# Optimization experiments

Measured on AMD Instinct MI355X. Metric: run time of the kernel, lower is better.

## Reference

```python
import jax, jax.numpy as jnp
import numpy as np

LN_EPS = 1e-5
NEG = -1e9


def _layernorm(x, g, b):
    m = jnp.mean(x, axis=-1, keepdims=True)
    v = jnp.mean(jnp.square(x - m), axis=-1, keepdims=True)
    return (x - m) * jax.lax.rsqrt(v + LN_EPS) * g + b


def setup_inputs() -> dict:
    key = jax.random.key(0)
    ks = jax.random.split(key, 16)
    B, S, E, H, D = 4, 2048, 1024, 16, 64
    s = 0.02
    return {
        "x": jax.random.normal(ks[0], (B, S, E), jnp.float32),
        "mask": jax.random.randint(ks[1], (B, S), 0, 2, jnp.int32),
        "Wq": jax.random.normal(ks[2], (H, E, D), jnp.float32) * s,
        "bq": jnp.zeros((H, D), jnp.float32),
        "Wk": jax.random.normal(ks[3], (H, E, D), jnp.float32) * s,
        "bk": jnp.zeros((H, D), jnp.float32),
        "Wv": jax.random.normal(ks[4], (H, E, D), jnp.float32) * s,
        "bv": jnp.zeros((H, D), jnp.float32),
        "Wo": jax.random.normal(ks[5], (H * D, E), jnp.float32) * s,
        "bo": jnp.zeros((E,), jnp.float32),
        "g1": jnp.ones((E,), jnp.float32),
        "b1": jnp.zeros((E,), jnp.float32),
        "W1": jax.random.normal(ks[6], (E, D), jnp.float32) * s,
        "c1": jnp.zeros((D,), jnp.float32),
        "W2": jax.random.normal(ks[7], (D, E), jnp.float32) * s,
        "c2": jnp.zeros((E,), jnp.float32),
        "g2": jnp.ones((E,), jnp.float32),
        "b2": jnp.zeros((E,), jnp.float32),
    }


def reference(x, mask, Wq, bq, Wk, bk, Wv, bv, Wo, bo, g1, b1, W1, c1, W2, c2, g2, b2):
    B, S, E = x.shape
    # per-head projections, batched over heads: [B,H,S,D]
    q = jnp.einsum('bse,hed->bhsd', x, Wq) + bq[None, :, None, :]
    k = jnp.einsum('bse,hed->bhsd', x, Wk) + bk[None, :, None, :]
    v = jnp.einsum('bse,hed->bhsd', x, Wv) + bv[None, :, None, :]
    # NOTE: original scales by sqrt(seq_len) (query.size(1)), not sqrt(head_dim)
    scale = jnp.asarray(S, x.dtype) ** 0.5
    scores = jnp.einsum('bhsd,bhtd->bhst', q, k) / scale
    scores = jnp.where(mask[:, None, None, :] == 0, NEG, scores)
    attn = jax.nn.softmax(scores, axis=-1)
    ctx = jnp.einsum('bhst,bhtd->bhsd', attn, v)
    # concat heads: [B,S,H*D]
    ctx = ctx.transpose(0, 2, 1, 3).reshape(B, S, -1)
    h = _layernorm(ctx @ Wo + bo, g1, b1)
    # bottleneck FFN (dropout = identity at eval), exact GELU
    f = jax.nn.gelu(h @ W1 + c1, approximate=False) @ W2 + c2
    # no residual connection in the original module
    return _layernorm(f, g2, b2)
```

## Files before the change

### kernel.cpp

```cpp
#include <hip/hip_runtime.h>
#include <math.h>

#define B_ 4
#define S_ 2048
#define E_ 1024
#define H_ 16
#define D_ 64
#define M_ (B_*S_)
#define QSCALE (0.022097086912079608f * 1.4426950408889634f)

typedef __bf16 bf16_t;
typedef __bf16 bf16x8 __attribute__((ext_vector_type(8)));
typedef float  f32x4  __attribute__((ext_vector_type(4)));

__device__ __forceinline__ void gload_lds16(const void* g, void* l) {
    __builtin_amdgcn_global_load_lds(
        (const __attribute__((address_space(1))) void*)g,
        (__attribute__((address_space(3))) void*)l, 16, 0, 0);
}
__device__ __forceinline__ bf16x8 ldsx8(const void* p) {
    return __builtin_bit_cast(bf16x8, *(const uint4*)p);
}
__device__ __forceinline__ unsigned short bf16bits(float x) {
    return __builtin_bit_cast(unsigned short, (bf16_t)x);
}
__device__ __forceinline__ int fk(int row) { return ((row & 3) + 2 * ((row >> 3) & 3)) & 7; }

template<int BM, int BN, int MODE>
__global__ __launch_bounds__(256) void gemm_bf16(
    const bf16_t* __restrict__ A, const bf16_t* __restrict__ Bt,
    bf16_t* __restrict__ ob0, bf16_t* __restrict__ ob1, bf16_t* __restrict__ ob2,
    const float* __restrict__ bias0, const float* __restrict__ bias1,
    const int* __restrict__ sidx, const int* __restrict__ nkv,
    int M, int N, int K)
{
    constexpr int FM = BM / 32, FN = BN / 32;
    __shared__ bf16_t As[BM * 64];
    __shared__ bf16_t Bs[BN * 64];

    const int tid = threadIdx.x;
    const int w   = tid >> 6;
    const int wr  = w >> 1, wc = w & 1;
    const int lr  = tid & 15;
    const int lg  = (tid >> 4) & 3;

    const int nwg  = gridDim.x * gridDim.y;
    int bidf = blockIdx.y * gridDim.x + blockIdx.x;
    bidf = (bidf & 7) * (nwg >> 3) + (bidf >> 3);
    const int bm = (bidf / gridDim.x) * BM;
    const int bn = (bidf % gridDim.x) * BN;

    int arow[FM];
    if constexpr (MODE == 2) {
        const int b2 = bm >> 11, rbase = bm & 2047;
        const int nkp128 = (nkv[b2] + 127) & ~127;
        if (rbase >= nkp128) return;
        #pragma unroll
        for (int i = 0; i < FM; ++i) {
            const int row = (i * 256 + tid) >> 3;
            arow[i] = (b2 << 11) + sidx[(b2 << 11) + rbase + row];
        }
    }

    f32x4 acc[FM][FN] = {};

    for (int kk = 0; kk < K; kk += 64) {
        __syncthreads();
        #pragma unroll
        for (int i = 0; i < BM / 32; ++i) {
            int idx = i * 256 + tid;
            int row = idx >> 3, slot = idx & 7;
            const size_t grow = (MODE == 2) ? (size_t)arow[i] : (size_t)(bm + row);
            gload_lds16(A + grow * K + kk + (slot ^ (row & 7)) * 8,
                        (char*)As + idx * 16);
        }
        #pragma unroll
        for (int i = 0; i < BN / 32; ++i) {
            int idx = i * 256 + tid;
            int row = idx >> 3, slot = idx & 7;
            gload_lds16(Bt + (size_t)(bn + row) * K + kk + (slot ^ (row & 7)) * 8,
                        (char*)Bs + idx * 16);
        }
        __syncthreads();

        #pragma unroll
        for (int h = 0; h < 2; ++h) {
            bf16x8 af[FM], bfr[FN];
            #pragma unroll
            for (int m = 0; m < FM; ++m) {
                int row = wr * (BM / 2) + m * 16 + lr;
                af[m] = ldsx8((char*)As + row * 128 + (((4 * h + lg) ^ (row & 7)) << 4));
            }
            #pragma unroll
            for (int n = 0; n < FN; ++n) {
                int col = wc * (BN / 2) + n * 16 + lr;
                bfr[n] = ldsx8((char*)Bs + col * 128 + (((4 * h + lg) ^ (col & 7)) << 4));
            }
            #pragma unroll
            for (int m = 0; m < FM; ++m)
                #pragma unroll
                for (int n = 0; n < FN; ++n)
                    acc[m][n] = __builtin_amdgcn_mfma_f32_16x16x32_bf16(
                        af[m], bfr[n], acc[m][n], 0, 0, 0);
        }
    }

    #pragma unroll
    for (int n = 0; n < FN; ++n) {
        const int gcol = bn + wc * (BN / 2) + n * 16 + lr;
        if constexpr (MODE == 2) {
            const int p = gcol >> 10, nn = gcol & 1023;
            const int b2 = bm >> 11;
            const float bvl = p ? bias1[nn] : bias0[nn];
            #pragma unroll
            for (int m = 0; m < FM; ++m) {
                const int ci0 = (bm & 2047) + wr * (BM / 2) + m * 16 + lg * 4;
                if (p) {
                    ushort4 o;
                    o.x = bf16bits(acc[m][n][0] + bvl);
                    o.y = bf16bits(acc[m][n][1] + bvl);
                    o.z = bf16bits(acc[m][n][2] + bvl);
                    o.w = bf16bits(acc[m][n][3] + bvl);
                    *(ushort4*)(ob2 + ((((size_t)b2 << 10) + nn) << 11) + ci0) = o;
                } else {
                    #pragma unroll
                    for (int r = 0; r < 4; ++r)
                        ob1[((size_t)((b2 << 11) + ci0 + r) << 10) + nn] =
                            (bf16_t)(acc[m][n][r] + bvl);
                }
            }
        } else {
            const float bvl = bias0[gcol];
            #pragma unroll
            for (int m = 0; m < FM; ++m)
                #pragma unroll
                for (int r = 0; r < 4; ++r) {
                    const int grow = bm + wr * (BM / 2) + m * 16 + lg * 4 + r;
                    float v = acc[m][n][r] + bvl;
                    if constexpr (MODE == 1)
                        v = 0.5f * v * (1.0f + erff(v * 0.70710678118654752f));
                    ob0[(size_t)grow * N + gcol] = (bf16_t)v;
                }
        }
    }
}

__global__ __launch_bounds__(256) void compact_mask(
    const int* __restrict__ mask, int* __restrict__ sidx, int* __restrict__ nkv)
{
    __shared__ int wsum[4];
    const int b = blockIdx.x;
    const int tid = threadIdx.x;
    const int lane = tid & 63, wv = tid >> 6;
    const int base = tid * 8;

    int m[8], loc[8];
    int cnt = 0;
    #pragma unroll
    for (int j = 0; j < 8; ++j) {
        m[j] = mask[b * S_ + base + j];
        loc[j] = cnt;
        cnt += (m[j] != 0);
    }
    int incl = cnt;
    #pragma unroll
    for (int off = 1; off < 64; off <<= 1) {
        int t = __shfl_up(incl, off);
        if (lane >= off) incl += t;
    }
    if (lane == 63) wsum[wv] = incl;
    const int excl_lane = incl - cnt;
    __syncthreads();
    int wbase = 0;
    for (int i = 0; i < wv; ++i) wbase += wsum[i];
    const int total = wsum[0] + wsum[1] + wsum[2] + wsum[3];
    if (tid == 0) nkv[b] = total;
    const int tbase = wbase + excl_lane;
    #pragma unroll
    for (int j = 0; j < 8; ++j)
        if (m[j]) sidx[b * S_ + tbase + loc[j]] = base + j;

    const int nkp = (total + 127) & ~127;
    for (int c = total + tid; c < nkp; c += 256)
        sidx[b * S_ + c] = 0;
}

__global__ __launch_bounds__(256) void attn_mfma(
    const bf16_t* __restrict__ qg, const bf16_t* __restrict__ kg,
    const bf16_t* __restrict__ vg, const int* __restrict__ nkv,
    bf16_t* __restrict__ ctx)
{
    __shared__ bf16_t ks[2][64 * 64];
    __shared__ bf16_t vts[2][64 * 64];

    const int tid = threadIdx.x;
    const int w   = tid >> 6;
    const int lr  = tid & 15;
    const int lg  = (tid >> 4) & 3;

    const int bid = blockIdx.x;
    const int xcd = bid & 7, kidx = bid >> 3;
    const int bh  = xcd * 8 + (kidx >> 4);
    const int xq  = kidx & 15;
    const int b   = bh >> 4, h = bh & 15;
    const int q0w = xq * 128 + w * 32;

    const int nk = nkv[b];
    const int ntiles = (nk + 63) >> 6;
    const bool hastail = (nk & 63) != 0;

    bf16x8 aq[2][2];
    #pragma unroll
    for (int f = 0; f < 2; ++f) {
        const bf16_t* qp = qg + ((size_t)(b * S_ + q0w + f * 16 + lr) << 10) + h * 64 + lg * 8;
        aq[f][0] = ldsx8(qp);
        aq[f][1] = ldsx8(qp + 32);
    }

    bf16x8 onesf;
    {
        bf16_t o1 = (bf16_t)((lr == 0) ? 1.0f : 0.0f);
        #pragma unroll
        for (int j = 0; j < 8; ++j) onesf[j] = o1;
    }

    int koff[2][2][2], voff[2][4];
    #pragma unroll
    for (int c = 0; c < 2; ++c) {
        #pragma unroll
        for (int kf1 = 0; kf1 < 2; ++kf1) {
            const int row = c * 32 + 8 * (lr >> 2) + 4 * kf1 + (lr & 3);
            const int f = fk(row);
            koff[c][kf1][0] = row * 128 + ((lg ^ f) << 4);
            koff[c][kf1][1] = row * 128 + (((4 + lg) ^ f) << 4);
        }
        #pragma unroll
        for (int n = 0; n < 4; ++n) {
            const int rowv = n * 16 + lr;
            voff[c][n] = rowv * 128 + (((4 * c + lg) ^ (rowv & 7)) << 4);
        }
    }

    const bf16_t* kptr[2];
    const bf16_t* vptr[2];
    char* kdst[2];
    char* vdst[2];
    #pragma unroll
    for (int it = 0; it < 2; ++it) {
        const int idx = it * 256 + tid;
        const int row = idx >> 3, slot = idx & 7;
        kptr[it] = kg + ((size_t)((b << 11) + row) << 10) + h * 64 + (slot ^ fk(row)) * 8;
        vptr[it] = vg + (((size_t)bh * 64 + row) << 11) + (slot ^ (row & 7)) * 8;
        kdst[it] = (char*)ks + idx * 16;
        vdst[it] = (char*)vts + idx * 16;
    }

    f32x4 accO[2][4] = {};
    f32x4 accL[2] = {};

    auto STAGE = [&](int buf) {
        const int nb = buf << 13;
        #pragma unroll
        for (int it = 0; it < 2; ++it) {
            gload_lds16(kptr[it], kdst[it] + nb);
            gload_lds16(vptr[it], vdst[it] + nb);
            kptr[it] += (size_t)64 << 10;
            vptr[it] += 64;
        }
    };

    auto COMPUTE = [&](int buf, int t0, bool tl) {
        const char* ksb = (const char*)ks + (buf << 13);
        const char* vsb = (const char*)vts + (buf << 13);
        #pragma unroll
        for (int c = 0; c < 2; ++c) {
            unsigned int pw0[4], pw1[4];
            #pragma unroll
            for (int kf1 = 0; kf1 < 2; ++kf1) {
                bf16x8 a0 = ldsx8(ksb + koff[c][kf1][0]);
                bf16x8 a1 = ldsx8(ksb + koff[c][kf1][1]);
                f32x4 z0 = {}, z1 = {};
                if (tl) {
                    const int keyb = t0 + c * 32 + 8 * lg + 4 * kf1;
                    f32x4 bias;
                    #pragma unroll
                    for (int r = 0; r < 4; ++r)
                        bias[r] = (keyb + r < nk) ? 0.0f : -1.0e9f;
                    z0 = bias; z1 = bias;
                }
                __builtin_amdgcn_s_setprio(1);
                z0 = __builtin_amdgcn_mfma_f32_16x16x32_bf16(a0, aq[0][0], z0, 0, 0, 0);
                z0 = __builtin_amdgcn_mfma_f32_16x16x32_bf16(a1, aq[0][1], z0, 0, 0, 0);
                z1 = __builtin_amdgcn_mfma_f32_16x16x32_bf16(a0, aq[1][0], z1, 0, 0, 0);
                z1 = __builtin_amdgcn_mfma_f32_16x16x32_bf16(a1, aq[1][1], z1, 0, 0, 0);
                __builtin_amdgcn_s_setprio(0);
                const float p00 = __builtin_amdgcn_exp2f(z0[0]);
                const float p01 = __builtin_amdgcn_exp2f(z0[1]);
                const float p02 = __builtin_amdgcn_exp2f(z0[2]);
                const float p03 = __builtin_amdgcn_exp2f(z0[3]);
                const float p10 = __builtin_amdgcn_exp2f(z1[0]);
                const float p11 = __builtin_amdgcn_exp2f(z1[1]);
                const float p12 = __builtin_amdgcn_exp2f(z1[2]);
                const float p13 = __builtin_amdgcn_exp2f(z1[3]);
                pw0[2 * kf1]     = bf16bits(p00) | ((unsigned)bf16bits(p01) << 16);
                pw0[2 * kf1 + 1] = bf16bits(p02) | ((unsigned)bf16bits(p03) << 16);
                pw1[2 * kf1]     = bf16bits(p10) | ((unsigned)bf16bits(p11) << 16);
                pw1[2 * kf1 + 1] = bf16bits(p12) | ((unsigned)bf16bits(p13) << 16);
            }
            uint4 pk0 = {pw0[0], pw0[1], pw0[2], pw0[3]};
            uint4 pk1 = {pw1[0], pw1[1], pw1[2], pw1[3]};
            const bf16x8 pa0 = __builtin_bit_cast(bf16x8, pk0);
            const bf16x8 pa1 = __builtin_bit_cast(bf16x8, pk1);

            __builtin_amdgcn_s_setprio(1);
            #pragma unroll
            for (int n = 0; n < 4; ++n) {
                bf16x8 av = ldsx8(vsb + voff[c][n]);
                accO[0][n] = __builtin_amdgcn_mfma_f32_16x16x32_bf16(av, pa0, accO[0][n], 0, 0, 0);
                accO[1][n] = __builtin_amdgcn_mfma_f32_16x16x32_bf16(av, pa1, accO[1][n], 0, 0, 0);
            }
            accL[0] = __builtin_amdgcn_mfma_f32_16x16x32_bf16(onesf, pa0, accL[0], 0, 0, 0);
            accL[1] = __builtin_amdgcn_mfma_f32_16x16x32_bf16(onesf, pa1, accL[1], 0, 0, 0);
            __builtin_amdgcn_s_setprio(0);
        }
    };

    STAGE(0);
    __syncthreads();

    int cur = 0;
    for (int t = 0; t < ntiles; ++t) {
        if (t + 1 < ntiles) STAGE(cur ^ 1);
        COMPUTE(cur, t * 64, hastail && (t == ntiles - 1));
        __syncthreads();
        cur ^= 1;
    }

    #pragma unroll
    for (int f = 0; f < 2; ++f) {
        const float inv = 1.0f / __shfl(accL[f][0], lr);
        bf16_t* obase = ctx + ((size_t)(b * S_ + q0w + f * 16 + lr) << 10) + h * 64;
        #pragma unroll
        for (int n = 0; n < 4; ++n) {
            ushort4 o;
            o.x = bf16bits(accO[f][n][0] * inv);
            o.y = bf16bits(accO[f][n][1] * inv);
            o.z = bf16bits(accO[f][n][2] * inv);
            o.w = bf16bits(accO[f][n][3] * inv);
            *(ushort4*)(obase + n * 16 + lg * 4) = o;
        }
    }
}

__global__ __launch_bounds__(256) void prep_all(
    const float* __restrict__ x, bf16_t* __restrict__ xb,
    const float* __restrict__ Wq, const float* __restrict__ Wk,
    const float* __restrict__ Wv, bf16_t* __restrict__ WqkvT,
    const float* __restrict__ Wo, bf16_t* __restrict__ WoT,
    const float* __restrict__ W1, bf16_t* __restrict__ W1T,
    const float* __restrict__ W2, bf16_t* __restrict__ W2T,
    const float* __restrict__ bq, float* __restrict__ bqs)
{
    __shared__ float t[32][33];
    const int tid = threadIdx.x;
    int bid = blockIdx.x;

    if (bid < 4096) {
        int i = bid * 256 + tid;
        float4 a = ((const float4*)x)[i * 2];
        float4 b = ((const float4*)x)[i * 2 + 1];
        unsigned int p0 = bf16bits(a.x) | ((unsigned)bf16bits(a.y) << 16);
        unsigned int p1 = bf16bits(a.z) | ((unsigned)bf16bits(a.w) << 16);
        unsigned int p2 = bf16bits(b.x) | ((unsigned)bf16bits(b.y) << 16);
        unsigned int p3 = bf16bits(b.z) | ((unsigned)bf16bits(b.w) << 16);
        uint4 o = {p0, p1, p2, p3};
        ((uint4*)xb)[i] = o;
        return;
    }
    bid -= 4096;

    if (bid == 4224) {
        #pragma unroll
        for (int j = 0; j < 4; ++j)
            bqs[tid * 4 + j] = bq[tid * 4 + j] * QSCALE;
        return;
    }

    const float* in; bf16_t* out;
    int R, C, c0, r0;
    float scale = 1.0f;
    if (bid < 3072) {
        const int p = bid >> 10, r = bid & 1023;
        const int z = r >> 6, rem = r & 63;
        in  = (p == 0 ? Wq : p == 1 ? Wk : Wv) + z * 65536;
        out = WqkvT + p * 1048576 + z * 65536;
        R = 1024; C = 64;
        c0 = (rem & 1) * 32; r0 = (rem >> 1) * 32;
        if (p == 0) scale = QSCALE;
    } else if (bid < 4096) {
        const int r = bid - 3072;
        in = Wo; out = WoT; R = 1024; C = 1024;
        c0 = (r & 31) * 32; r0 = (r >> 5) * 32;
    } else if (bid < 4160) {
        const int r = bid - 4096;
        in = W1; out = W1T; R = 1024; C = 64;
        c0 = (r & 1) * 32; r0 = (r >> 1) * 32;
    } else {
        const int r = bid - 4160;
        in = W2; out = W2T; R = 64; C = 1024;
        c0 = (r & 31) * 32; r0 = (r >> 5) * 32;
    }

    {
        int rr = tid >> 3, c4 = (tid & 7) * 4;
        float4 v = *(const float4*)&in[(size_t)(r0 + rr) * C + c0 + c4];
        t[rr][c4 + 0] = v.x * scale;
        t[rr][c4 + 1] = v.y * scale;
        t[rr][c4 + 2] = v.z * scale;
        t[rr][c4 + 3] = v.w * scale;
    }
    __syncthreads();
    {
        int c = tid >> 3, r4 = (tid & 7) * 4;
        ushort4 o;
        o.x = bf16bits(t[r4 + 0][c]);
        o.y = bf16bits(t[r4 + 1][c]);
        o.z = bf16bits(t[r4 + 2][c]);
        o.w = bf16bits(t[r4 + 3][c]);
        *(ushort4*)(out + (size_t)(c0 + c) * R + r0 + r4) = o;
    }
}

template<typename InT, typename OutT>
__global__ __launch_bounds__(256) void ln_kernel(
    const InT* __restrict__ in, const float* __restrict__ g,
    const float* __restrict__ bta, OutT* __restrict__ out)
{
    const int row = blockIdx.x;
    const int tid = threadIdx.x;

    float x0, x1, x2, x3;
    if constexpr (sizeof(InT) == 4) {
        float4 xv = ((const float4*)(in + (size_t)row * E_))[tid];
        x0 = xv.x; x1 = xv.y; x2 = xv.z; x3 = xv.w;
    } else {
        ushort4 xv = *(const ushort4*)((const bf16_t*)in + (size_t)row * E_ + tid * 4);
        x0 = (float)__builtin_bit_cast(bf16_t, xv.x);
        x1 = (float)__builtin_bit_cast(bf16_t, xv.y);
        x2 = (float)__builtin_bit_cast(bf16_t, xv.z);
        x3 = (float)__builtin_bit_cast(bf16_t, xv.w);
    }
    float s  = x0 + x1 + x2 + x3;
    float sq = x0 * x0 + x1 * x1 + x2 * x2 + x3 * x3;
    #pragma unroll
    for (int off = 32; off > 0; off >>= 1) {
        s  += __shfl_down(s, off);
        sq += __shfl_down(sq, off);
    }
    __shared__ float ss[4], ssq[4];
    if ((tid & 63) == 0) { ss[tid >> 6] = s; ssq[tid >> 6] = sq; }
    __syncthreads();
    s  = ss[0] + ss[1] + ss[2] + ss[3];
    sq = ssq[0] + ssq[1] + ssq[2] + ssq[3];

    const float mean = s * (1.0f / E_);
    const float var  = sq * (1.0f / E_) - mean * mean;
    const float rstd = rsqrtf(var + 1e-5f);

    float4 gv = ((const float4*)g)[tid];
    float4 bv = ((const float4*)bta)[tid];
    float o0 = (x0 - mean) * rstd * gv.x + bv.x;
    float o1 = (x1 - mean) * rstd * gv.y + bv.y;
    float o2 = (x2 - mean) * rstd * gv.z + bv.z;
    float o3 = (x3 - mean) * rstd * gv.w + bv.w;
    if constexpr (sizeof(OutT) == 4) {
        float4 o = {o0, o1, o2, o3};
        ((float4*)((float*)out + (size_t)row * E_))[tid] = o;
    } else {
        ushort4 o;
        o.x = bf16bits(o0); o.y = bf16bits(o1);
        o.z = bf16bits(o2); o.w = bf16bits(o3);
        *(ushort4*)((bf16_t*)out + (size_t)row * E_ + tid * 4) = o;
    }
}

extern "C" void kernel_launch(void* const* d_in, const int* in_sizes, int n_in,
                              void* d_out, int out_size, void* d_ws, size_t ws_size,
                              hipStream_t stream)
{
    const float* x    = (const float*)d_in[0];
    const int*   mask = (const int*)d_in[1];
    const float* Wq   = (const float*)d_in[2];
    const float* bq   = (const float*)d_in[3];
    const float* Wk   = (const float*)d_in[4];
    const float* bk   = (const float*)d_in[5];
    const float* Wv   = (const float*)d_in[6];
    const float* bv   = (const float*)d_in[7];
    const float* Wo   = (const float*)d_in[8];
    const float* bo   = (const float*)d_in[9];
    const float* g1   = (const float*)d_in[10];
    const float* b1   = (const float*)d_in[11];
    const float* W1   = (const float*)d_in[12];
    const float* c1   = (const float*)d_in[13];
    const float* W2   = (const float*)d_in[14];
    const float* c2   = (const float*)d_in[15];
    const float* g2   = (const float*)d_in[16];
    const float* b2   = (const float*)d_in[17];

    char* W = (char*)d_ws;
    bf16_t* xb    = (bf16_t*)(W + 0);
    bf16_t* WqkvT = (bf16_t*)(W + 16777216);
    bf16_t* WoT   = (bf16_t*)(W + 23068672);
    bf16_t* W1T   = (bf16_t*)(W + 25165824);
    bf16_t* W2T   = (bf16_t*)(W + 25296896);
    bf16_t* qbuf  = (bf16_t*)(W + 25427968);
    bf16_t* kbuf  = (bf16_t*)(W + 42205184);
    bf16_t* vtc   = (bf16_t*)(W + 58982400);
    bf16_t* ctx   = (bf16_t*)(W + 75759616);
    bf16_t* t1b   = (bf16_t*)(W + 25427968);
    bf16_t* hb    = (bf16_t*)(W + 42205184);
    bf16_t* f1b   = (bf16_t*)(W + 0);
    bf16_t* f2b   = (bf16_t*)(W + 58982400);
    int*    sidx  = (int*)(W + 92536832);
    int*    nkv   = (int*)(W + 92569600);
    float*  bqs   = (float*)(W + 92569664);
    float*  out   = (float*)d_out;

    prep_all<<<8321, 256, 0, stream>>>(x, xb, Wq, Wk, Wv, WqkvT,
                                       Wo, WoT, W1, W1T, W2, W2T, bq, bqs);

    compact_mask<<<4, 256, 0, stream>>>(mask, sidx, nkv);

    gemm_bf16<128, 128, 0><<<dim3(8, 64), 256, 0, stream>>>(
        xb, WqkvT, qbuf, nullptr, nullptr, bqs, nullptr, nullptr, nullptr,
        M_, 1024, 1024);

    gemm_bf16<128, 128, 2><<<dim3(16, 64), 256, 0, stream>>>(
        xb, WqkvT + (1 << 20), nullptr, kbuf, vtc, bk, bv, sidx, nkv,
        M_, 2048, 1024);

    attn_mfma<<<dim3(1024), 256, 0, stream>>>(qbuf, kbuf, vtc, nkv, ctx);

    gemm_bf16<128, 128, 0><<<dim3(8, 64), 256, 0, stream>>>(
        ctx, WoT, t1b, nullptr, nullptr, bo, nullptr, nullptr, nullptr,
        M_, 1024, 1024);

    ln_kernel<bf16_t, bf16_t><<<8192, 256, 0, stream>>>(t1b, g1, b1, hb);

    gemm_bf16<32, 64, 1><<<dim3(1, 256), 256, 0, stream>>>(
        hb, W1T, f1b, nullptr, nullptr, c1, nullptr, nullptr, nullptr,
        M_, 64, 1024);

    gemm_bf16<128, 128, 0><<<dim3(8, 64), 256, 0, stream>>>(
        f1b, W2T, f2b, nullptr, nullptr, c2, nullptr, nullptr, nullptr,
        M_, 1024, 64);

    ln_kernel<bf16_t, float><<<8192, 256, 0, stream>>>(f2b, g2, b2, out);
}
```

Measured before the change: 210.6 us.

## Double-buffer GEMM LDS loads and merge Q and KV projections into one launch

The GEMM kernel gets two LDS buffers. The next K-tile is prefetched with global_load_lds while the current tile is computed, using explicit vmcnt waits and raw s_barrier instead of __syncthreads. The separate Q and compacted-KV projection launches are merged into one MODE 3 launch that dispatches by block index, which cuts a launch and lets both parts fill the device together. The attention loop gets the same explicit partial-wait barrier scheme. The costs are twice the LDS footprint in the GEMM, which may lower occupancy, and hand-counted vmcnt values that must match the number of issued loads.

```diff
diff --git a/kernel.cpp b/kernel.cpp
--- a/kernel.cpp
+++ b/kernel.cpp
@@ -24,6 +24,12 @@
 __device__ __forceinline__ unsigned short bf16bits(float x) {
     return __builtin_bit_cast(unsigned short, (bf16_t)x);
 }
+template<int N> __device__ __forceinline__ void waitv() {
+    if constexpr (N == 8)      asm volatile("s_waitcnt vmcnt(8) lgkmcnt(0)" ::: "memory");
+    else if constexpr (N == 4) asm volatile("s_waitcnt vmcnt(4) lgkmcnt(0)" ::: "memory");
+    else if constexpr (N == 3) asm volatile("s_waitcnt vmcnt(3) lgkmcnt(0)" ::: "memory");
+    else                       asm volatile("s_waitcnt vmcnt(0) lgkmcnt(0)" ::: "memory");
+}
 __device__ __forceinline__ int fk(int row) { return ((row & 3) + 2 * ((row >> 3) & 3)) & 7; }
 
 template<int BM, int BN, int MODE>
@@ -31,12 +37,14 @@
     const bf16_t* __restrict__ A, const bf16_t* __restrict__ Bt,
     bf16_t* __restrict__ ob0, bf16_t* __restrict__ ob1, bf16_t* __restrict__ ob2,
     const float* __restrict__ bias0, const float* __restrict__ bias1,
+    const float* __restrict__ bias2,
     const int* __restrict__ sidx, const int* __restrict__ nkv,
     int M, int N, int K)
 {
     constexpr int FM = BM / 32, FN = BN / 32;
-    __shared__ bf16_t As[BM * 64];
-    __shared__ bf16_t Bs[BN * 64];
+    constexpr int NL = BM / 32 + BN / 32;
+    __shared__ bf16_t As[2][BM * 64];
+    __shared__ bf16_t Bs[2][BN * 64];
 
     const int tid = threadIdx.x;
     const int w   = tid >> 6;
@@ -47,54 +55,79 @@
     const int nwg  = gridDim.x * gridDim.y;
     int bidf = blockIdx.y * gridDim.x + blockIdx.x;
     bidf = (bidf & 7) * (nwg >> 3) + (bidf >> 3);
-    const int bm = (bidf / gridDim.x) * BM;
-    const int bn = (bidf % gridDim.x) * BN;
+
+    int bm, bn;
+    bool isQ = true;
+    const bf16_t* Bp = Bt;
+    if constexpr (MODE == 3) {
+        isQ = bidf < 512;
+        if (isQ) {
+            bm = (bidf >> 3) * 128;
+            bn = (bidf & 7) * 128;
+        } else {
+            const int kv = bidf - 512;
+            bm = (kv >> 4) * 128;
+            bn = (kv & 15) * 128;
+            Bp = Bt + (1 << 20);
+        }
+    } else {
+        bm = (bidf / gridDim.x) * BM;
+        bn = (bidf % gridDim.x) * BN;
+    }
 
     int arow[FM];
-    if constexpr (MODE == 2) {
-        const int b2 = bm >> 11, rbase = bm & 2047;
-        const int nkp128 = (nkv[b2] + 127) & ~127;
-        if (rbase >= nkp128) return;
-        #pragma unroll
-        for (int i = 0; i < FM; ++i) {
-            const int row = (i * 256 + tid) >> 3;
-            arow[i] = (b2 << 11) + sidx[(b2 << 11) + rbase + row];
+    {
+        if constexpr (MODE == 3) {
+            const int b2 = bm >> 11, rbase = bm & 2047;
+            if (!isQ) {
+                const int nkp128 = (nkv[b2] + 127) & ~127;
+                if (rbase >= nkp128) return;
+            }
+            #pragma unroll
+            for (int i = 0; i < FM; ++i) {
+                const int row = (i * 256 + tid) >> 3;
+                arow[i] = isQ ? (bm + row)
+                              : ((b2 << 11) + sidx[(b2 << 11) + rbase + row]);
+            }
+        } else {
+            #pragma unroll
+            for (int i = 0; i < FM; ++i)
+                arow[i] = bm + ((i * 256 + tid) >> 3);
         }
     }
 
     f32x4 acc[FM][FN] = {};
 
-    for (int kk = 0; kk < K; kk += 64) {
-        __syncthreads();
+    auto STAGE = [&](int buf, int kk) {
         #pragma unroll
         for (int i = 0; i < BM / 32; ++i) {
             int idx = i * 256 + tid;
             int row = idx >> 3, slot = idx & 7;
-            const size_t grow = (MODE == 2) ? (size_t)arow[i] : (size_t)(bm + row);
-            gload_lds16(A + grow * K + kk + (slot ^ (row & 7)) * 8,
-                        (char*)As + idx * 16);
+            gload_lds16(A + (size_t)arow[i] * K + kk + (slot ^ (row & 7)) * 8,
+                        (char*)As[buf] + idx * 16);
         }
         #pragma unroll
         for (int i = 0; i < BN / 32; ++i) {
             int idx = i * 256 + tid;
             int row = idx >> 3, slot = idx & 7;
-            gload_lds16(Bt + (size_t)(bn + row) * K + kk + (slot ^ (row & 7)) * 8,
-                        (char*)Bs + idx * 16);
-        }
-        __syncthreads();
-
+            gload_lds16(Bp + (size_t)(bn + row) * K + kk + (slot ^ (row & 7)) * 8,
+                        (char*)Bs[buf] + idx * 16);
+        }
+    };
+
+    auto COMPUTE = [&](int buf) {
         #pragma unroll
         for (int h = 0; h < 2; ++h) {
             bf16x8 af[FM], bfr[FN];
             #pragma unroll
             for (int m = 0; m < FM; ++m) {
                 int row = wr * (BM / 2) + m * 16 + lr;
-                af[m] = ldsx8((char*)As + row * 128 + (((4 * h + lg) ^ (row & 7)) << 4));
+                af[m] = ldsx8((char*)As[buf] + row * 128 + (((4 * h + lg) ^ (row & 7)) << 4));
             }
             #pragma unroll
             for (int n = 0; n < FN; ++n) {
                 int col = wc * (BN / 2) + n * 16 + lr;
-                bfr[n] = ldsx8((char*)Bs + col * 128 + (((4 * h + lg) ^ (col & 7)) << 4));
+                bfr[n] = ldsx8((char*)Bs[buf] + col * 128 + (((4 * h + lg) ^ (col & 7)) << 4));
             }
             #pragma unroll
             for (int m = 0; m < FM; ++m)
@@ -103,33 +136,62 @@
                     acc[m][n] = __builtin_amdgcn_mfma_f32_16x16x32_bf16(
                         af[m], bfr[n], acc[m][n], 0, 0, 0);
         }
+    };
+
+    STAGE(0, 0);
+    int cur = 0;
+    for (int kk = 0; kk < K; kk += 64) {
+        const bool hasnext = (kk + 64 < K);
+        if (hasnext) {
+            STAGE(cur ^ 1, kk + 64);
+            waitv<NL>();
+        } else {
+            waitv<0>();
+        }
+        __builtin_amdgcn_s_barrier();
+        COMPUTE(cur);
+        __builtin_amdgcn_s_barrier();
+        cur ^= 1;
     }
 
     #pragma unroll
     for (int n = 0; n < FN; ++n) {
-        const int gcol = bn + wc * (BN / 2) + n * 16 + lr;
-        if constexpr (MODE == 2) {
-            const int p = gcol >> 10, nn = gcol & 1023;
-            const int b2 = bm >> 11;
-            const float bvl = p ? bias1[nn] : bias0[nn];
-            #pragma unroll
-            for (int m = 0; m < FM; ++m) {
-                const int ci0 = (bm & 2047) + wr * (BM / 2) + m * 16 + lg * 4;
-                if (p) {
-                    ushort4 o;
-                    o.x = bf16bits(acc[m][n][0] + bvl);
-                    o.y = bf16bits(acc[m][n][1] + bvl);
-                    o.z = bf16bits(acc[m][n][2] + bvl);
-                    o.w = bf16bits(acc[m][n][3] + bvl);
-                    *(ushort4*)(ob2 + ((((size_t)b2 << 10) + nn) << 11) + ci0) = o;
-                } else {
+        if constexpr (MODE == 3) {
+            if (isQ) {
+                const int gcol = bn + wc * 64 + n * 16 + lr;
+                const float bvl = bias0[gcol];
+                #pragma unroll
+                for (int m = 0; m < FM; ++m)
                     #pragma unroll
-                    for (int r = 0; r < 4; ++r)
-                        ob1[((size_t)((b2 << 11) + ci0 + r) << 10) + nn] =
-                            (bf16_t)(acc[m][n][r] + bvl);
+                    for (int r = 0; r < 4; ++r) {
+                        const int grow = bm + wr * 64 + m * 16 + lg * 4 + r;
+                        ob0[((size_t)grow << 10) + gcol] = (bf16_t)(acc[m][n][r] + bvl);
+                    }
+            } else {
+                const int gcol = bn + wc * 64 + n * 16 + lr;
+                const int p = gcol >> 10, nn = gcol & 1023;
+                const int b2 = bm >> 11;
+                const float bvl = p ? bias2[nn] : bias1[nn];
+                #pragma unroll
+                for (int m = 0; m < FM; ++m) {
+                    const int ci0 = (bm & 2047) + wr * 64 + m * 16 + lg * 4;
+                    if (p) {
+                        ushort4 o;
+                        o.x = bf16bits(acc[m][n][0] + bvl);
+                        o.y = bf16bits(acc[m][n][1] + bvl);
+                        o.z = bf16bits(acc[m][n][2] + bvl);
+                        o.w = bf16bits(acc[m][n][3] + bvl);
+                        *(ushort4*)(ob2 + ((((size_t)b2 << 10) + nn) << 11) + ci0) = o;
+                    } else {
+                        #pragma unroll
+                        for (int r = 0; r < 4; ++r)
+                            ob1[((size_t)((b2 << 11) + ci0 + r) << 10) + nn] =
+                                (bf16_t)(acc[m][n][r] + bvl);
+                    }
                 }
             }
         } else {
+            const int gcol = bn + wc * (BN / 2) + n * 16 + lr;
             const float bvl = bias0[gcol];
             #pragma unroll
             for (int m = 0; m < FM; ++m)
@@ -326,13 +388,17 @@
     };
 
     STAGE(0);
-    __syncthreads();
-
     int cur = 0;
     for (int t = 0; t < ntiles; ++t) {
-        if (t + 1 < ntiles) STAGE(cur ^ 1);
+        if (t + 1 < ntiles) {
+            STAGE(cur ^ 1);
+            waitv<4>();
+        } else {
+            waitv<0>();
+        }
+        __builtin_amdgcn_s_barrier();
         COMPUTE(cur, t * 64, hastail && (t == ntiles - 1));
-        __syncthreads();
+        __builtin_amdgcn_s_barrier();
         cur ^= 1;
     }
 
@@ -531,28 +597,23 @@
 
     compact_mask<<<4, 256, 0, stream>>>(mask, sidx, nkv);
 
+    gemm_bf16<128, 128, 3><<<dim3(1536), 256, 0, stream>>>(
+        xb, WqkvT, qbuf, kbuf, vtc, bqs, bk, bv, sidx, nkv, M_, 1024, 1024);
+
+    attn_mfma<<<dim3(1024), 256, 0, stream>>>(qbuf, kbuf, vtc, nkv, ctx);
+
     gemm_bf16<128, 128, 0><<<dim3(8, 64), 256, 0, stream>>>(
-        xb, WqkvT, qbuf, nullptr, nullptr, bqs, nullptr, nullptr, nullptr,
+        ctx, WoT, t1b, nullptr, nullptr, bo, nullptr, nullptr, nullptr, nullptr,
         M_, 1024, 1024);
 
-    gemm_bf16<128, 128, 2><<<dim3(16, 64), 256, 0, stream>>>(
-        xb, WqkvT + (1 << 20), nullptr, kbuf, vtc, bk, bv, sidx, nkv,
-        M_, 2048, 1024);
-
-    attn_mfma<<<dim3(1024), 256, 0, stream>>>(qbuf, kbuf, vtc, nkv, ctx);
+    ln_kernel<bf16_t, bf16_t><<<8192, 256, 0, stream>>>(t1b, g1, b1, hb);
+
+    gemm_bf16<32, 64, 1><<<dim3(1, 256), 256, 0, stream>>>(
+        hb, W1T, f1b, nullptr, nullptr, c1, nullptr, nullptr, nullptr, nullptr,
+        M_, 64, 1024);
 
     gemm_bf16<128, 128, 0><<<dim3(8, 64), 256, 0, stream>>>(
-        ctx, WoT, t1b, nullptr, nullptr, bo, nullptr, nullptr, nullptr,
-        M_, 1024, 1024);
-
-    ln_kernel<bf16_t, bf16_t><<<8192, 256, 0, stream>>>(t1b, g1, b1, hb);
-
-    gemm_bf16<32, 64, 1><<<dim3(1, 256), 256, 0, stream>>>(
-        hb, W1T, f1b, nullptr, nullptr, c1, nullptr, nullptr, nullptr,
-        M_, 64, 1024);
-
-    gemm_bf16<128, 128, 0><<<dim3(8, 64), 256, 0, stream>>>(
-        f1b, W2T, f2b, nullptr, nullptr, c2, nullptr, nullptr, nullptr,
+        f1b, W2T, f2b, nullptr, nullptr, c2, nullptr, nullptr, nullptr, nullptr,
         M_, 1024, 64);
 
     ln_kernel<bf16_t, float><<<8192, 256, 0, stream>>>(f2b, g2, b2, out);
```

After: 199.7 us. -5.2%, faster.
